# Optimization experiments

Hardware: AMD Instinct MI355X
Metric: run time of the kernel (lower is better)

The kernel has to match this reference:

```python
import jax, jax.numpy as jnp
import numpy as np

B, T, C = 4, 2048, 1024
NH = 16
HD = C // NH  # 64


def setup_inputs() -> dict:
    key = jax.random.key(0)
    k1, k2, k3, k4, k5 = jax.random.split(key, 5)
    s_in = 1.0 / np.sqrt(C)
    return {
        "x": jax.random.normal(k1, (B, T, C), dtype=jnp.float32),
        "attention_mask": jnp.ones((B, T), dtype=jnp.float32),
        "W_qkv": jax.random.normal(k2, (C, 3 * C), dtype=jnp.float32) * s_in,
        "b_qkv": jnp.zeros((3 * C,), dtype=jnp.float32),
        "W_out": jax.random.normal(k3, (C, C), dtype=jnp.float32) * s_in,
        "b_out": jnp.zeros((C,), dtype=jnp.float32),
    }


def reference(x, attention_mask, W_qkv, b_qkv, W_out, b_out):
    Bx, Tx, Cx = x.shape
    # QKV projection: (B,T,3C)
    qkv = x @ W_qkv + b_qkv
    Q, K, V = jnp.split(qkv, 3, axis=-1)
    # (B, NH, T, HD)
    Q = Q.reshape(Bx, Tx, NH, HD).transpose(0, 2, 1, 3)
    K = K.reshape(Bx, Tx, NH, HD).transpose(0, 2, 1, 3)
    V = V.reshape(Bx, Tx, NH, HD).transpose(0, 2, 1, 3)
    # scaled scores (B, NH, T, T)
    scores = jnp.einsum("bhqd,bhkd->bhqk", Q, K) * (1.0 / np.sqrt(HD))
    # causal mask: set strictly-upper triangle to -inf (mask-fill semantics)
    causal = jnp.tril(jnp.ones((Tx, Tx), dtype=bool))[None, None]
    scores = jnp.where(causal, scores, -jnp.inf)
    # additive padding mask
    pad = (1.0 - attention_mask)[:, None, None, :] * jnp.finfo(scores.dtype).min
    scores = scores + pad
    attn = jax.nn.softmax(scores, axis=-1)
    # weighted values -> (B, T, C)
    wv = jnp.einsum("bhqk,bhkd->bhqd", attn, V)
    wv = wv.transpose(0, 2, 1, 3).reshape(Bx, Tx, Cx)
    return wv @ W_out + b_out
```

## Files before the change

kernel.cpp:

```cpp
#include <hip/hip_runtime.h>
#include <math.h>

constexpr int BB = 4;
constexpr int TT = 2048;
constexpr int CC = 1024;
constexpr int NHH = 16;
constexpr int HDD = 64;
constexpr int C3 = 3 * CC;

typedef __bf16 bf16x8 __attribute__((ext_vector_type(8)));
typedef float  f32x4  __attribute__((ext_vector_type(4)));

__device__ __forceinline__ unsigned short f2bf(float x) {
    union { float f; unsigned u; } v; v.f = x;
    unsigned r = v.u + 0x7fffu + ((v.u >> 16) & 1u);
    return (unsigned short)(r >> 16);
}

#define AS1(p) ((const __attribute__((address_space(1))) void*)(p))
#define AS3(p) ((__attribute__((address_space(3))) void*)(p))

constexpr float SM2 = 17.312340490667561f;

constexpr int CAST_BLOCKS = (BB * TT * CC / 4) / 256;
constexpr int TQKV_BLOCKS = (C3 / 64) * (CC / 64);
constexpr int TOUT_BLOCKS = (CC / 64) * (CC / 64);
constexpr int KB_BLOCKS   = (BB * TT) / 256;

__global__ __launch_bounds__(256) void prep(
    const float* __restrict__ x,
    const float* __restrict__ Wqkv,
    const float* __restrict__ Wout,
    const float* __restrict__ amask,
    unsigned short* __restrict__ xb,
    unsigned short* __restrict__ Wqkvt,
    unsigned short* __restrict__ Woutt,
    float* __restrict__ kbias)
{
    __shared__ float tile[64][65];
    const int bid = blockIdx.x;
    const int t = threadIdx.x;

    if (bid < CAST_BLOCKS) {
        const int i = bid * 256 + t;
        float4 v = ((const float4*)x)[i];
        ushort4 o;
        o.x = f2bf(v.x); o.y = f2bf(v.y); o.z = f2bf(v.z); o.w = f2bf(v.w);
        ((ushort4*)xb)[i] = o;
        return;
    }
    if (bid >= CAST_BLOCKS + TQKV_BLOCKS + TOUT_BLOCKS) {
        const int i = (bid - CAST_BLOCKS - TQKV_BLOCKS - TOUT_BLOCKS) * 256 + t;
        kbias[i] = (amask[i] - 1.0f) * 1.0e38f - SM2;
        return;
    }

    const float* src; unsigned short* dst; int R, Cn, r0, c0;
    if (bid < CAST_BLOCKS + TQKV_BLOCKS) {
        const int tb = bid - CAST_BLOCKS;
        src = Wqkv; dst = Wqkvt; R = CC; Cn = C3;
        c0 = (tb % (C3 / 64)) * 64; r0 = (tb / (C3 / 64)) * 64;
    } else {
        const int tb = bid - CAST_BLOCKS - TQKV_BLOCKS;
        src = Wout; dst = Woutt; R = CC; Cn = CC;
        c0 = (tb % (CC / 64)) * 64; r0 = (tb / (CC / 64)) * 64;
    }

    const int lr = t >> 4, lc = (t & 15) * 4;
    #pragma unroll
    for (int s = 0; s < 4; ++s) {
        float4 v = *(const float4*)&src[(size_t)(r0 + lr + s * 16) * Cn + c0 + lc];
        tile[lr + s * 16][lc + 0] = v.x;
        tile[lr + s * 16][lc + 1] = v.y;
        tile[lr + s * 16][lc + 2] = v.z;
        tile[lr + s * 16][lc + 3] = v.w;
    }
    __syncthreads();
    const int oi = t >> 2, oc = (t & 3) * 16;
    unsigned short buf[16];
    #pragma unroll
    for (int u = 0; u < 16; ++u)
        buf[u] = f2bf(tile[oc + u][oi]);
    unsigned short* d = &dst[(size_t)(c0 + oi) * R + r0 + oc];
    *(uint4*)(d + 0) = *(uint4*)&buf[0];
    *(uint4*)(d + 8) = *(uint4*)&buf[8];
}

template<bool VSPLIT>
__global__ __launch_bounds__(256, 2) void gemm_bt_mfma(
    const unsigned short* __restrict__ A,
    const unsigned short* __restrict__ Bt,
    const float* __restrict__ bias,
    float* __restrict__ OutF,
    unsigned short* __restrict__ Qp,
    unsigned short* __restrict__ Kp,
    unsigned short* __restrict__ Vtp,
    int M, int N, int K, float qscale)
{
    __shared__ alignas(16) unsigned short As[2][128 * 64];
    __shared__ alignas(16) unsigned short Bs[2][128 * 64];

    const int tid  = threadIdx.x;
    const int w    = tid >> 6;
    const int lane = tid & 63;
    const int quad = lane >> 4;
    const int col  = lane & 15;

    const int nX  = gridDim.x;
    const int lin = blockIdx.y * nX + blockIdx.x;
    const int pos = lin >> 3;
    const int mt  = ((lin & 7) << 3) | (pos & 7);
    const int nt  = pos >> 3;
    const int m0 = mt * 128, n0 = nt * 128;
    const int wr = w >> 1, wc = w & 1;

    f32x4 acc[4][4];
    #pragma unroll
    for (int i = 0; i < 4; ++i)
        #pragma unroll
        for (int j = 0; j < 4; ++j)
            #pragma unroll
            for (int r = 0; r < 4; ++r)
                acc[i][j][r] = 0.0f;

    const int srow = tid >> 3;
    const int spos = tid & 7;
    char* AsB = (char*)&As[0][0];
    char* BsB = (char*)&Bs[0][0];

    const int nk = K >> 6;

    auto DMA = [&](int kt, int buf) {
        const int k0 = kt << 6;
        #pragma unroll
        for (int i = 0; i < 4; ++i) {
            const int row = srow + 32 * i;
            const int sch = spos ^ (row & 7);
            __builtin_amdgcn_global_load_lds(
                AS1(A + (size_t)(m0 + row) * K + k0 + sch * 8),
                AS3(AsB + buf * 16384 + i * 4096 + w * 1024), 16, 0, 0);
            __builtin_amdgcn_global_load_lds(
                AS1(Bt + (size_t)(n0 + row) * K + k0 + sch * 8),
                AS3(BsB + buf * 16384 + i * 4096 + w * 1024), 16, 0, 0);
        }
    };

    DMA(0, 0);
    DMA(1, 1);
    asm volatile("s_waitcnt vmcnt(8)" ::: "memory");
    __builtin_amdgcn_s_barrier();

    for (int kt = 0; kt < nk; ++kt) {
        const int cur = kt & 1;
        const unsigned short* as = &As[cur][0];
        const unsigned short* bs = &Bs[cur][0];

        #pragma unroll
        for (int ks = 0; ks < 2; ++ks) {
            bf16x8 af[4], bf[4];
            #pragma unroll
            for (int i = 0; i < 4; ++i) {
                const int ra = wr * 64 + i * 16 + col;
                const int pa = ((quad + ks * 4) ^ (ra & 7)) * 8;
                af[i] = *(const bf16x8*)&as[ra * 64 + pa];
                const int rb = wc * 64 + i * 16 + col;
                const int pb = ((quad + ks * 4) ^ (rb & 7)) * 8;
                bf[i] = *(const bf16x8*)&bs[rb * 64 + pb];
            }
            #pragma unroll
            for (int i = 0; i < 4; ++i)
                #pragma unroll
                for (int j = 0; j < 4; ++j)
                    acc[i][j] = __builtin_amdgcn_mfma_f32_16x16x32_bf16(af[i], bf[j], acc[i][j], 0, 0, 0);
        }

        __builtin_amdgcn_s_barrier();
        if (kt + 2 < nk) {
            DMA(kt + 2, cur);
            asm volatile("s_waitcnt vmcnt(8)" ::: "memory");
        } else {
            asm volatile("s_waitcnt vmcnt(0)" ::: "memory");
        }
        __builtin_amdgcn_s_barrier();
    }

    if (VSPLIT) {
        if (n0 < CC) {
            #pragma unroll
            for (int i = 0; i < 4; ++i)
                #pragma unroll
                for (int r = 0; r < 4; ++r) {
                    const int m = m0 + wr * 64 + i * 16 + quad * 4 + r;
                    #pragma unroll
                    for (int j = 0; j < 4; ++j) {
                        const int n = n0 + wc * 64 + j * 16 + col;
                        Qp[(size_t)m * CC + n] = f2bf((acc[i][j][r] + bias[n]) * qscale);
                    }
                }
        } else if (n0 < 2 * CC) {
            #pragma unroll
            for (int i = 0; i < 4; ++i) {
                const int mb   = m0 + wr * 64 + i * 16 + quad * 4;
                const int bidx = mb >> 11;
                const int tloc = mb & 2047;
                #pragma unroll
                for (int j = 0; j < 4; ++j) {
                    const int n  = n0 + wc * 64 + j * 16 + col;
                    const int hh = (n - CC) >> 6;
                    const int dd = (n - CC) & 63;
                    #pragma unroll
                    for (int r = 0; r < 4; ++r)
                        Kp[(((size_t)bidx * NHH + hh) * TT + tloc + r) * HDD + dd] =
                            f2bf(acc[i][j][r] + bias[n]);
                }
            }
        } else {
            #pragma unroll
            for (int i = 0; i < 4; ++i) {
                const int mb   = m0 + wr * 64 + i * 16 + quad * 4;
                const int bidx = mb >> 11;
                const int tloc = mb & 2047;
                const int ktile = tloc >> 6, tc = tloc & 63;
                #pragma unroll
                for (int j = 0; j < 4; ++j) {
                    const int n  = n0 + wc * 64 + j * 16 + col;
                    const int hh = (n - 2 * CC) >> 6;
                    const int dd = (n - 2 * CC) & 63;
                    unsigned short pk[4];
                    #pragma unroll
                    for (int r = 0; r < 4; ++r)
                        pk[r] = f2bf(acc[i][j][r] + bias[n]);
                    *(uint2*)&Vtp[((((size_t)bidx * NHH + hh) * 32 + ktile) * HDD + dd) * 64 + tc] =
                        *(const uint2*)pk;
                }
            }
        }
    } else {
        #pragma unroll
        for (int i = 0; i < 4; ++i)
            #pragma unroll
            for (int r = 0; r < 4; ++r) {
                const int m = m0 + wr * 64 + i * 16 + quad * 4 + r;
                #pragma unroll
                for (int j = 0; j < 4; ++j) {
                    const int n = n0 + wc * 64 + j * 16 + col;
                    OutF[(size_t)m * N + n] = acc[i][j][r] + bias[n];
                }
            }
    }
}

constexpr int PP = 72;

__global__ __launch_bounds__(256, 3) void attn_mfma(
    const unsigned short* __restrict__ Qp,
    const unsigned short* __restrict__ Kp,
    const unsigned short* __restrict__ Vtp,
    const float* __restrict__ kbias,
    unsigned short* __restrict__ WV)
{
    __shared__ alignas(16) unsigned short Ks [2][64 * 64];
    __shared__ alignas(16) unsigned short Vts[2][64 * 64];
    __shared__ alignas(16) __bf16        Ps[4][32 * PP];

    const int tid  = threadIdx.x;
    const int w    = tid >> 6;
    const int lane = tid & 63;
    const int quad = lane >> 4;
    const int col  = lane & 15;

    const int gi = blockIdx.x;
    const int j  = gi >> 3;
    const int bh = ((gi & 7) << 3) | (j & 7);
    const int qb = 15 - (j >> 3);
    const int b = bh >> 4, h = bh & 15;

    const unsigned short* Qg = Qp + (size_t)b * TT * CC + (size_t)h * HDD;
    const unsigned short* Kg = Kp + (size_t)bh * TT * HDD;
    const unsigned short* Vg = Vtp + (size_t)bh * 32 * HDD * 64;
    const float* kb_g = kbias + b * TT;

    const int srow = tid >> 3;
    const int sch  = (tid & 7) ^ (srow & 7);
    char* KsB  = (char*)&Ks[0][0];
    char* VtsB = (char*)&Vts[0][0];

    const int qw = qb * 128 + w * 32;
    const int ntiles = 2 * qb + 2;

    bf16x8 qfa0 = *(const bf16x8*)(Qg + (size_t)(qw + col) * CC + quad * 8);
    bf16x8 qfa1 = *(const bf16x8*)(Qg + (size_t)(qw + col) * CC + 32 + quad * 8);
    bf16x8 qfb0 = *(const bf16x8*)(Qg + (size_t)(qw + 16 + col) * CC + quad * 8);
    bf16x8 qfb1 = *(const bf16x8*)(Qg + (size_t)(qw + 16 + col) * CC + 32 + quad * 8);

    f32x4 o[2][4];
    float l[2][4];
    #pragma unroll
    for (int hh = 0; hh < 2; ++hh)
        #pragma unroll
        for (int t = 0; t < 4; ++t)
            #pragma unroll
            for (int r = 0; r < 4; ++r) o[hh][t][r] = 0.0f;
    #pragma unroll
    for (int hh = 0; hh < 2; ++hh)
        #pragma unroll
        for (int r = 0; r < 4; ++r) l[hh][r] = 0.0f;

    auto DMA = [&](int tile, int buf) {
        #pragma unroll
        for (int i = 0; i < 2; ++i) {
            __builtin_amdgcn_global_load_lds(
                AS1(Kg + (size_t)(tile * 64 + srow + 32 * i) * HDD + sch * 8),
                AS3(KsB + buf * 8192 + i * 4096 + w * 1024), 16, 0, 0);
            __builtin_amdgcn_global_load_lds(
                AS1(Vg + ((size_t)tile * 64 + srow + 32 * i) * 64 + sch * 8),
                AS3(VtsB + buf * 8192 + i * 4096 + w * 1024), 16, 0, 0);
        }
    };

    float kbc[4], kbn[4];
    DMA(0, 0);
    #pragma unroll
    for (int t = 0; t < 4; ++t) kbc[t] = kb_g[t * 16 + col];
    DMA(1, 1);
    #pragma unroll
    for (int t = 0; t < 4; ++t) kbn[t] = kb_g[64 + t * 16 + col];
    asm volatile("s_waitcnt vmcnt(8)" ::: "memory");
    __builtin_amdgcn_s_barrier();

    for (int it = 0; it < ntiles; ++it) {
        const int kt  = it << 6;
        const int cur = it & 1;

        if (kt <= qw + 31) {
            const unsigned short* ksb = &Ks[cur][0];
            const unsigned short* vsb = &Vts[cur][0];

            f32x4 s[2][4];
            #pragma unroll
            for (int t = 0; t < 4; ++t) {
                const int row = t * 16 + col;
                const int c0 = (quad ^ (row & 7)) * 8;
                const int c1 = ((quad + 4) ^ (row & 7)) * 8;
                bf16x8 k0 = *(const bf16x8*)&ksb[row * 64 + c0];
                bf16x8 k1 = *(const bf16x8*)&ksb[row * 64 + c1];
                f32x4 z;
                #pragma unroll
                for (int r = 0; r < 4; ++r) z[r] = kbc[t];
                f32x4 za = __builtin_amdgcn_mfma_f32_16x16x32_bf16(qfa0, k0, z, 0, 0, 0);
                za = __builtin_amdgcn_mfma_f32_16x16x32_bf16(qfa1, k1, za, 0, 0, 0);
                s[0][t] = za;
                f32x4 zb = __builtin_amdgcn_mfma_f32_16x16x32_bf16(qfb0, k0, z, 0, 0, 0);
                zb = __builtin_amdgcn_mfma_f32_16x16x32_bf16(qfb1, k1, zb, 0, 0, 0);
                s[1][t] = zb;
            }

            const bool needc = (kt + 64 > qw);
            #pragma unroll
            for (int hh = 0; hh < 2; ++hh)
                #pragma unroll
                for (int t = 0; t < 4; ++t) {
                    const int key = kt + t * 16 + col;
                    #pragma unroll
                    for (int r = 0; r < 4; ++r) {
                        float p = __builtin_amdgcn_exp2f(s[hh][t][r]);
                        if (needc && key > qw + hh * 16 + quad * 4 + r) p = 0.0f;
                        l[hh][r] += p;
                        Ps[w][(hh * 16 + quad * 4 + r) * PP + t * 16 + col] = (__bf16)p;
                    }
                }

            bf16x8 p0a = *(const bf16x8*)&Ps[w][col * PP + quad * 8];
            bf16x8 p1a = *(const bf16x8*)&Ps[w][col * PP + 32 + quad * 8];
            bf16x8 p0b = *(const bf16x8*)&Ps[w][(16 + col) * PP + quad * 8];
            bf16x8 p1b = *(const bf16x8*)&Ps[w][(16 + col) * PP + 32 + quad * 8];
            #pragma unroll
            for (int t = 0; t < 4; ++t) {
                const int row = t * 16 + col;
                const int c0 = (quad ^ (row & 7)) * 8;
                const int c1 = ((quad + 4) ^ (row & 7)) * 8;
                bf16x8 v0 = *(const bf16x8*)&vsb[row * 64 + c0];
                bf16x8 v1 = *(const bf16x8*)&vsb[row * 64 + c1];
                o[0][t] = __builtin_amdgcn_mfma_f32_16x16x32_bf16(p0a, v0, o[0][t], 0, 0, 0);
                o[0][t] = __builtin_amdgcn_mfma_f32_16x16x32_bf16(p1a, v1, o[0][t], 0, 0, 0);
                o[1][t] = __builtin_amdgcn_mfma_f32_16x16x32_bf16(p0b, v0, o[1][t], 0, 0, 0);
                o[1][t] = __builtin_amdgcn_mfma_f32_16x16x32_bf16(p1b, v1, o[1][t], 0, 0, 0);
            }
        }

        __builtin_amdgcn_s_barrier();

        #pragma unroll
        for (int t = 0; t < 4; ++t) kbc[t] = kbn[t];

        if (it + 2 < ntiles) {
            DMA(it + 2, cur);
            #pragma unroll
            for (int t = 0; t < 4; ++t)
                kbn[t] = kb_g[(it + 2) * 64 + t * 16 + col];
            asm volatile("s_waitcnt vmcnt(8)" ::: "memory");
        } else {
            asm volatile("s_waitcnt vmcnt(0)" ::: "memory");
        }
        __builtin_amdgcn_s_barrier();
    }

    #pragma unroll
    for (int hh = 0; hh < 2; ++hh) {
        #pragma unroll
        for (int off = 1; off < 16; off <<= 1)
            #pragma unroll
            for (int r = 0; r < 4; ++r)
                l[hh][r] += __shfl_xor(l[hh][r], off);
        #pragma unroll
        for (int r = 0; r < 4; ++r) {
            const float inv = 1.0f / l[hh][r];
            const int q = qw + hh * 16 + quad * 4 + r;
            unsigned short* dst = WV + ((size_t)b * TT + q) * CC + (size_t)h * HDD;
            #pragma unroll
            for (int t = 0; t < 4; ++t)
                dst[t * 16 + col] = f2bf(o[hh][t][r] * inv);
        }
    }
}

extern "C" void kernel_launch(void* const* d_in, const int* in_sizes, int n_in,
                              void* d_out, int out_size, void* d_ws, size_t ws_size,
                              hipStream_t stream) {
    const float* x     = (const float*)d_in[0];
    const float* amask = (const float*)d_in[1];
    const float* Wqkv  = (const float*)d_in[2];
    const float* bqkv  = (const float*)d_in[3];
    const float* Wout  = (const float*)d_in[4];
    const float* bout  = (const float*)d_in[5];
    float* out = (float*)d_out;

    const int M = BB * TT;

    unsigned short* xb    = (unsigned short*)d_ws;
    unsigned short* Wqkvt = xb    + (size_t)M * CC;
    unsigned short* Woutt = Wqkvt + (size_t)C3 * CC;
    unsigned short* Qp    = Woutt + (size_t)CC * CC;
    unsigned short* Kp    = Qp    + (size_t)M * CC;
    unsigned short* Vtp   = Kp    + (size_t)M * CC;
    unsigned short* wvb   = Vtp   + (size_t)M * CC;
    float*          kbias = (float*)(wvb + (size_t)M * CC);

    dim3 blk(256);

    prep<<<dim3(CAST_BLOCKS + TQKV_BLOCKS + TOUT_BLOCKS + KB_BLOCKS), blk, 0, stream>>>(
        x, Wqkv, Wout, amask, xb, Wqkvt, Woutt, kbias);

    gemm_bt_mfma<true><<<dim3(C3 / 128, M / 128), blk, 0, stream>>>(
        xb, Wqkvt, bqkv, nullptr, Qp, Kp, Vtp, M, C3, CC, 0.18033688011112043f);
    attn_mfma<<<dim3(1024), dim3(256), 0, stream>>>(
        Qp, Kp, Vtp, kbias, wvb);
    gemm_bt_mfma<false><<<dim3(CC / 128, M / 128), blk, 0, stream>>>(
        wvb, Woutt, bout, out, nullptr, nullptr, nullptr, M, CC, CC, 1.0f);
}
```

Baseline: 238.1 us.

## Add dedicated 256x192-tile QKV GEMM kernel with XCD-aware block mapping

Replaces the generic 128x128-tile QKV projection GEMM with a dedicated kernel using 512 threads and 256x192 output tiles. This raises arithmetic intensity per LDS load and cuts the grid to 512 blocks. Block indices are remapped so each XCD works on a contiguous set of M tiles, which should improve L2 reuse of the A operand. In exchange the kernel uses larger accumulators and more LDS (about 112KB per block), which may limit occupancy and register headroom.

```diff
diff --git a/kernel.cpp b/kernel.cpp
--- a/kernel.cpp
+++ b/kernel.cpp
@@ -21,6 +21,7 @@
 #define AS3(p) ((__attribute__((address_space(3))) void*)(p))
 
 constexpr float SM2 = 17.312340490667561f;
+constexpr float QSCALE = 0.18033688011112043f;
 
 constexpr int CAST_BLOCKS = (BB * TT * CC / 4) / 256;
 constexpr int TQKV_BLOCKS = (C3 / 64) * (CC / 64);
@@ -86,6 +87,143 @@
     *(uint4*)(d + 8) = *(uint4*)&buf[8];
 }
 
+__global__ __launch_bounds__(512, 2) void gemm_qkv(
+    const unsigned short* __restrict__ A,
+    const unsigned short* __restrict__ Bt,
+    const float* __restrict__ bias,
+    unsigned short* __restrict__ Qp,
+    unsigned short* __restrict__ Kp,
+    unsigned short* __restrict__ Vtp)
+{
+    __shared__ alignas(16) unsigned short As[2][256 * 64];
+    __shared__ alignas(16) unsigned short Bs[2][192 * 64];
+
+    const int tid  = threadIdx.x;
+    const int w    = tid >> 6;
+    const int lane = tid & 63;
+    const int quad = lane >> 4;
+    const int col  = lane & 15;
+    const int wr = w >> 2, wc = w & 3;
+
+    const int lin = blockIdx.x;
+    const int xcd = lin & 7, idx = lin >> 3;
+    const int mt = xcd * 4 + (idx & 3);
+    const int nt = idx >> 2;
+    const int m0 = mt * 256, n0 = nt * 192;
+
+    f32x4 acc[8][3];
+    #pragma unroll
+    for (int i = 0; i < 8; ++i)
+        #pragma unroll
+        for (int j = 0; j < 3; ++j)
+            #pragma unroll
+            for (int r = 0; r < 4; ++r)
+                acc[i][j][r] = 0.0f;
+
+    const int srow = tid >> 3;
+    const int spos = tid & 7;
+    const int sch  = spos ^ (srow & 7);
+    char* AsB = (char*)&As[0][0];
+    char* BsB = (char*)&Bs[0][0];
+
+    constexpr int K  = CC;
+    constexpr int nk = K / 64;
+
+    auto DMA = [&](int kt, int buf) {
+        const int k0 = kt << 6;
+        #pragma unroll
+        for (int i = 0; i < 4; ++i)
+            __builtin_amdgcn_global_load_lds(
+                AS1(A + (size_t)(m0 + srow + 64 * i) * K + k0 + sch * 8),
+                AS3(AsB + buf * 32768 + i * 8192 + w * 1024), 16, 0, 0);
+        #pragma unroll
+        for (int i = 0; i < 3; ++i)
+            __builtin_amdgcn_global_load_lds(
+                AS1(Bt + (size_t)(n0 + srow + 64 * i) * K + k0 + sch * 8),
+                AS3(BsB + buf * 24576 + i * 8192 + w * 1024), 16, 0, 0);
+    };
+
+    DMA(0, 0);
+    DMA(1, 1);
+    asm volatile("s_waitcnt vmcnt(7)" ::: "memory");
+    __builtin_amdgcn_s_barrier();
+
+    for (int kt = 0; kt < nk; ++kt) {
+        const int cur = kt & 1;
+        const unsigned short* as = &As[cur][0];
+        const unsigned short* bs = &Bs[cur][0];
+
+        #pragma unroll
+        for (int ks = 0; ks < 2; ++ks) {
+            bf16x8 af[8], bf[3];
+            #pragma unroll
+            for (int i = 0; i < 8; ++i) {
+                const int ra = wr * 128 + i * 16 + col;
+                af[i] = *(const bf16x8*)&as[ra * 64 + ((quad + ks * 4) ^ (col & 7)) * 8];
+            }
+            #pragma unroll
+            for (int j = 0; j < 3; ++j) {
+                const int rb = wc * 48 + j * 16 + col;
+                bf[j] = *(const bf16x8*)&bs[rb * 64 + ((quad + ks * 4) ^ (col & 7)) * 8];
+            }
+            #pragma unroll
+            for (int i = 0; i < 8; ++i)
+                #pragma unroll
+                for (int j = 0; j < 3; ++j)
+                    acc[i][j] = __builtin_amdgcn_mfma_f32_16x16x32_bf16(af[i], bf[j], acc[i][j], 0, 0, 0);
+        }
+
+        __builtin_amdgcn_s_barrier();
+        if (kt + 2 < nk) {
+            DMA(kt + 2, cur);
+            asm volatile("s_waitcnt vmcnt(7)" ::: "memory");
+        } else {
+            asm volatile("s_waitcnt vmcnt(0)" ::: "memory");
+        }
+        __builtin_amdgcn_s_barrier();
+    }
+
+    #pragma unroll
+    for (int j = 0; j < 3; ++j) {
+        const int n = n0 + wc * 48 + j * 16 + col;
+        const float bn = bias[n];
+        if (n < CC) {
+            #pragma unroll
+            for (int i = 0; i < 8; ++i) {
+                const int mb = m0 + wr * 128 + i * 16 + quad * 4;
+                #pragma unroll
+                for (int r = 0; r < 4; ++r)
+                    Qp[(size_t)(mb + r) * CC + n] = f2bf((acc[i][j][r] + bn) * QSCALE);
+            }
+        } else if (n < 2 * CC) {
+            const int hh = (n - CC) >> 6, dd = (n - CC) & 63;
+            #pragma unroll
+            for (int i = 0; i < 8; ++i) {
+                const int mb = m0 + wr * 128 + i * 16 + quad * 4;
+                const int bidx = mb >> 11, tloc = mb & 2047;
+                #pragma unroll
+                for (int r = 0; r < 4; ++r)
+                    Kp[(((size_t)bidx * NHH + hh) * TT + tloc + r) * HDD + dd] =
+                        f2bf(acc[i][j][r] + bn);
+            }
+        } else {
+            const int hh = (n - 2 * CC) >> 6, dd = (n - 2 * CC) & 63;
+            #pragma unroll
+            for (int i = 0; i < 8; ++i) {
+                const int mb = m0 + wr * 128 + i * 16 + quad * 4;
+                const int bidx = mb >> 11, tloc = mb & 2047;
+                const int ktile = tloc >> 6, tc = tloc & 63;
+                unsigned short pk[4];
+                #pragma unroll
+                for (int r = 0; r < 4; ++r)
+                    pk[r] = f2bf(acc[i][j][r] + bn);
+                *(uint2*)&Vtp[((((size_t)bidx * NHH + hh) * 32 + ktile) * HDD + dd) * 64 + tc] =
+                    *(const uint2*)pk;
+            }
+        }
+    }
+}
+
 template<bool VSPLIT>
 __global__ __launch_bounds__(256, 2) void gemm_bt_mfma(
     const unsigned short* __restrict__ A,
@@ -185,56 +323,6 @@
     }
 
     if (VSPLIT) {
-        if (n0 < CC) {
-            #pragma unroll
-            for (int i = 0; i < 4; ++i)
-                #pragma unroll
-                for (int r = 0; r < 4; ++r) {
-                    const int m = m0 + wr * 64 + i * 16 + quad * 4 + r;
-                    #pragma unroll
-                    for (int j = 0; j < 4; ++j) {
-                        const int n = n0 + wc * 64 + j * 16 + col;
-                        Qp[(size_t)m * CC + n] = f2bf((acc[i][j][r] + bias[n]) * qscale);
-                    }
-                }
-        } else if (n0 < 2 * CC) {
-            #pragma unroll
-            for (int i = 0; i < 4; ++i) {
-                const int mb   = m0 + wr * 64 + i * 16 + quad * 4;
-                const int bidx = mb >> 11;
-                const int tloc = mb & 2047;
-                #pragma unroll
-                for (int j = 0; j < 4; ++j) {
-                    const int n  = n0 + wc * 64 + j * 16 + col;
-                    const int hh = (n - CC) >> 6;
-                    const int dd = (n - CC) & 63;
-                    #pragma unroll
-                    for (int r = 0; r < 4; ++r)
-                        Kp[(((size_t)bidx * NHH + hh) * TT + tloc + r) * HDD + dd] =
-                            f2bf(acc[i][j][r] + bias[n]);
-                }
-            }
-        } else {
-            #pragma unroll
-            for (int i = 0; i < 4; ++i) {
-                const int mb   = m0 + wr * 64 + i * 16 + quad * 4;
-                const int bidx = mb >> 11;
-                const int tloc = mb & 2047;
-                const int ktile = tloc >> 6, tc = tloc & 63;
-                #pragma unroll
-                for (int j = 0; j < 4; ++j) {
-                    const int n  = n0 + wc * 64 + j * 16 + col;
-                    const int hh = (n - 2 * CC) >> 6;
-                    const int dd = (n - 2 * CC) & 63;
-                    unsigned short pk[4];
-                    #pragma unroll
-                    for (int r = 0; r < 4; ++r)
-                        pk[r] = f2bf(acc[i][j][r] + bias[n]);
-                    *(uint2*)&Vtp[((((size_t)bidx * NHH + hh) * 32 + ktile) * HDD + dd) * 64 + tc] =
-                        *(const uint2*)pk;
-                }
-            }
-        }
     } else {
         #pragma unroll
         for (int i = 0; i < 4; ++i)
@@ -451,8 +539,8 @@
     prep<<<dim3(CAST_BLOCKS + TQKV_BLOCKS + TOUT_BLOCKS + KB_BLOCKS), blk, 0, stream>>>(
         x, Wqkv, Wout, amask, xb, Wqkvt, Woutt, kbias);
 
-    gemm_bt_mfma<true><<<dim3(C3 / 128, M / 128), blk, 0, stream>>>(
-        xb, Wqkvt, bqkv, nullptr, Qp, Kp, Vtp, M, C3, CC, 0.18033688011112043f);
+    gemm_qkv<<<dim3(512), dim3(512), 0, stream>>>(
+        xb, Wqkvt, bqkv, Qp, Kp, Vtp);
     attn_mfma<<<dim3(1024), dim3(256), 0, stream>>>(
         Qp, Kp, Vtp, kbias, wvb);
     gemm_bt_mfma<false><<<dim3(CC / 128, M / 128), blk, 0, stream>>>(
```

Result: slower. 247.6 us (+4.0%).
